# Kernel optimization log

Measured on AMD Instinct MI355X. Metric: run time of the kernel, lower is better.

## Reference

```python
import jax, jax.numpy as jnp
import numpy as np

KSIZE = 5

def _sigmas(ksize, sigma_color, sigma_space):
    if sigma_space == 0:
        sigma_space = 0.15 * ksize + 0.35
    if sigma_color == 0:
        sigma_color = sigma_space
    return sigma_color, sigma_space

def _space_kernel(ksize, sigma):
    # matches getGaussianKernel (sigma > 0 branch)
    xs = jnp.arange(ksize, dtype=jnp.float32) - ksize // 2
    k1 = jnp.exp(-xs**2 / (2.0 * sigma * sigma))
    k2 = k1[:, None] * k1[None, :]
    return k2 / k2.sum()

def bilateral(x, ksize, sigma_color, sigma_space):
    sigma_color, sigma_space = _sigmas(ksize, sigma_color, sigma_space)
    pad = (ksize - 1) // 2
    B, C, H, W = x.shape
    xp = jnp.pad(x, ((0, 0), (0, 0), (pad, pad), (pad, pad)), mode='reflect')
    # patches[b,c,h,w,ki,kj] == padded[b,c,h+ki,w+kj] (same layout as torch unfold)
    patches = jnp.stack(
        [xp[:, :, i:i + H, j:j + W] for i in range(ksize) for j in range(ksize)],
        axis=-1,
    ).reshape(B, C, H, W, ksize, ksize)
    diff = patches - x[..., None, None]
    w_color = jnp.exp(-diff**2 / (2.0 * sigma_color * sigma_color))
    w_color = w_color / w_color.sum(axis=(-1, -2), keepdims=True)
    w_space = _space_kernel(ksize, sigma_space)  # [k,k], broadcasts
    w = w_color * w_space
    return (w * patches).sum(axis=(-1, -2)) / w.sum(axis=(-1, -2))

def setup_inputs() -> dict:
    key = jax.random.key(0)
    x = jax.random.uniform(key, (16, 3, 512, 512), dtype=jnp.float32)
    return {"x": x}

def reference(x):
    return bilateral(x, KSIZE, 0.0, 0.0)
```

## Files before the change

kernel.cpp:

```cpp
#include <hip/hip_runtime.h>


constexpr int H_ = 512;
constexpr int W_ = 512;

__global__ __launch_bounds__(256) void bilateral_kernel(
    const float* __restrict__ x,
    float* __restrict__ out,
    int nquads)
{
    int t = blockIdx.x * 256 + threadIdx.x;
    if (t >= nquads) return;

    int w0   = (t & 127) << 2;
    int row  = t >> 7;
    int h    = row & (H_ - 1);
    int pbase = (row - h) * W_;

    const float coef2 = -0.59615498f;

    int rb[5];
#pragma unroll
    for (int i = 0; i < 5; ++i) {
        int r = h + i - 2;
        r = min(abs(r), 2 * (H_ - 1) - r);
        rb[i] = pbase + r * W_;
    }

    int aL = max(w0 - 2, 0);
    int aR = min(w0 + 4, W_ - 2);
    bool bL = (w0 == 0);
    bool bR = (w0 == W_ - 4);

    float4 cc = *(const float4*)(x + rb[2] + w0);
    float c[4] = {cc.x, cc.y, cc.z, cc.w};

    float num[4] = {0.f, 0.f, 0.f, 0.f};
    float den[4] = {0.f, 0.f, 0.f, 0.f};

#pragma unroll
    for (int i = 0; i < 5; ++i) {
        const float* rp = x + rb[i];
        float2 l2 = *(const float2*)(rp + aL);
        float4 c4 = *(const float4*)(rp + w0);
        float2 r2 = *(const float2*)(rp + aR);
        float Wf[8] = {l2.x, l2.y, c4.x, c4.y, c4.z, c4.w, r2.x, r2.y};
        Wf[0] = bL ? Wf[4] : Wf[0];
        Wf[7] = bR ? Wf[3] : Wf[7];

#pragma unroll
        for (int q = 0; q < 4; ++q) {
            float cq = c[q];
#pragma unroll
            for (int j = 0; j < 5; ++j) {
                float p = Wf[q + j];
                float d = p - cq;
                float sij = (float)((i - 2) * (i - 2) + (j - 2) * (j - 2));
                float arg = fmaf(d, d, sij) * coef2;
                float wgt = __builtin_amdgcn_exp2f(arg);
                num[q] = fmaf(wgt, p, num[q]);
                den[q] += wgt;
            }
        }
    }

    float4 o;
    o.x = num[0] * __builtin_amdgcn_rcpf(den[0]);
    o.y = num[1] * __builtin_amdgcn_rcpf(den[1]);
    o.z = num[2] * __builtin_amdgcn_rcpf(den[2]);
    o.w = num[3] * __builtin_amdgcn_rcpf(den[3]);
    *(float4*)(out + rb[2] + w0) = o;
}

extern "C" void kernel_launch(void* const* d_in, const int* in_sizes, int n_in,
                              void* d_out, int out_size, void* d_ws, size_t ws_size,
                              hipStream_t stream)
{
    const float* x = (const float*)d_in[0];
    float* out = (float*)d_out;
    int nquads = in_sizes[0] >> 2;
    int blocks = (nquads + 255) / 256;
    bilateral_kernel<<<blocks, 256, 0, stream>>>(x, out, nquads);
}
```

Before: 138.5 us.

## Compute a 4x4 output tile per thread, reusing an 8x8 register window

Each thread now produces a 4x4 block of outputs instead of a 1x4 strip. It loads an 8x8 window of the input into registers once, which cuts redundant row loads from 5 per output row to 2 per output row. The spatial coefficient is folded so that each tap costs one FMA before the exp. The change raises register pressure (64 window values) and uses a launch-bounds occupancy hint, and it cuts the thread count by four, which may reduce latency hiding on a compute-bound kernel.

```diff
diff --git a/kernel.cpp b/kernel.cpp
--- a/kernel.cpp
+++ b/kernel.cpp
@@ -4,72 +4,75 @@
 constexpr int H_ = 512;
 constexpr int W_ = 512;
 
-__global__ __launch_bounds__(256) void bilateral_kernel(
+__global__ __launch_bounds__(256, 3) void bilateral_kernel(
     const float* __restrict__ x,
     float* __restrict__ out,
-    int nquads)
+    int nthreads)
 {
     int t = blockIdx.x * 256 + threadIdx.x;
-    if (t >= nquads) return;
+    if (t >= nthreads) return;
 
-    int w0   = (t & 127) << 2;
-    int row  = t >> 7;
-    int h    = row & (H_ - 1);
-    int pbase = (row - h) * W_;
-
-    const float coef2 = -0.59615498f;
-
-    int rb[5];
-#pragma unroll
-    for (int i = 0; i < 5; ++i) {
-        int r = h + i - 2;
-        r = min(abs(r), 2 * (H_ - 1) - r);
-        rb[i] = pbase + r * W_;
-    }
+    int qx = t & 127;
+    int rg = (t >> 7) & 127;
+    int pl = t >> 14;
+    int w0 = qx << 2;
+    int h0 = rg << 2;
+    const float* plane = x + ((long)pl << 18);
+    float* oplane = out + ((long)pl << 18);
 
     int aL = max(w0 - 2, 0);
     int aR = min(w0 + 4, W_ - 2);
     bool bL = (w0 == 0);
     bool bR = (w0 == W_ - 4);
 
-    float4 cc = *(const float4*)(x + rb[2] + w0);
-    float c[4] = {cc.x, cc.y, cc.z, cc.w};
-
-    float num[4] = {0.f, 0.f, 0.f, 0.f};
-    float den[4] = {0.f, 0.f, 0.f, 0.f};
-
+    float Wn[8][8];
 #pragma unroll
-    for (int i = 0; i < 5; ++i) {
-        const float* rp = x + rb[i];
+    for (int k = 0; k < 8; ++k) {
+        int r = h0 + k - 2;
+        r = min(abs(r), 2 * (H_ - 1) - r);
+        const float* rp = plane + r * W_;
         float2 l2 = *(const float2*)(rp + aL);
         float4 c4 = *(const float4*)(rp + w0);
         float2 r2 = *(const float2*)(rp + aR);
-        float Wf[8] = {l2.x, l2.y, c4.x, c4.y, c4.z, c4.w, r2.x, r2.y};
-        Wf[0] = bL ? Wf[4] : Wf[0];
-        Wf[7] = bR ? Wf[3] : Wf[7];
+        Wn[k][2] = c4.x; Wn[k][3] = c4.y; Wn[k][4] = c4.z; Wn[k][5] = c4.w;
+        Wn[k][0] = bL ? c4.z : l2.x;
+        Wn[k][1] = l2.y;
+        Wn[k][6] = r2.x;
+        Wn[k][7] = bR ? c4.y : r2.y;
+    }
+
+    const float coef2 = -0.59615498f;
 
 #pragma unroll
+    for (int oi = 0; oi < 4; ++oi) {
+        float num[4] = {0.f, 0.f, 0.f, 0.f};
+        float den[4] = {0.f, 0.f, 0.f, 0.f};
+#pragma unroll
         for (int q = 0; q < 4; ++q) {
-            float cq = c[q];
+            float c = Wn[oi + 2][q + 2];
 #pragma unroll
-            for (int j = 0; j < 5; ++j) {
-                float p = Wf[q + j];
-                float d = p - cq;
-                float sij = (float)((i - 2) * (i - 2) + (j - 2) * (j - 2));
-                float arg = fmaf(d, d, sij) * coef2;
-                float wgt = __builtin_amdgcn_exp2f(arg);
-                num[q] = fmaf(wgt, p, num[q]);
-                den[q] += wgt;
+            for (int di = 0; di < 5; ++di) {
+#pragma unroll
+                for (int dj = 0; dj < 5; ++dj) {
+                    float p = Wn[oi + di][q + dj];
+                    float cs = coef2 * (float)((di - 2) * (di - 2) +
+                                               (dj - 2) * (dj - 2));
+                    float d = p - c;
+                    float e = d * coef2;
+                    float arg = fmaf(e, d, cs);
+                    float w = __builtin_amdgcn_exp2f(arg);
+                    num[q] = fmaf(w, p, num[q]);
+                    den[q] += w;
+                }
             }
         }
+        float4 o;
+        o.x = num[0] * __builtin_amdgcn_rcpf(den[0]);
+        o.y = num[1] * __builtin_amdgcn_rcpf(den[1]);
+        o.z = num[2] * __builtin_amdgcn_rcpf(den[2]);
+        o.w = num[3] * __builtin_amdgcn_rcpf(den[3]);
+        *(float4*)(oplane + (h0 + oi) * W_ + w0) = o;
     }
-
-    float4 o;
-    o.x = num[0] * __builtin_amdgcn_rcpf(den[0]);
-    o.y = num[1] * __builtin_amdgcn_rcpf(den[1]);
-    o.z = num[2] * __builtin_amdgcn_rcpf(den[2]);
-    o.w = num[3] * __builtin_amdgcn_rcpf(den[3]);
-    *(float4*)(out + rb[2] + w0) = o;
 }
 
 extern "C" void kernel_launch(void* const* d_in, const int* in_sizes, int n_in,
@@ -78,7 +81,7 @@
 {
     const float* x = (const float*)d_in[0];
     float* out = (float*)d_out;
-    int nquads = in_sizes[0] >> 2;
-    int blocks = (nquads + 255) / 256;
-    bilateral_kernel<<<blocks, 256, 0, stream>>>(x, out, nquads);
+    int nthreads = in_sizes[0] >> 4;
+    int blocks = (nthreads + 255) / 256;
+    bilateral_kernel<<<blocks, 256, 0, stream>>>(x, out, nthreads);
 }
```

Result: no change. 137.2 us (-0.9%).
